# Performance work log

Measured on AMD Instinct MI355X. Metric: run time of the kernel, lower is better.

Reference implementation:

```python
import jax, jax.numpy as jnp
import numpy as np

EMBED_DIM = 1024
NUM_HEADS = 16
HEAD_DIM = EMBED_DIM // NUM_HEADS
B, S = 2, 2048


def setup_inputs() -> dict:
    key = jax.random.key(0)
    ks = jax.random.split(key, 12)
    sd = 1.0 / np.sqrt(EMBED_DIM)
    def lin(kw, kb):
        W = jax.random.uniform(kw, (EMBED_DIM, EMBED_DIM), jnp.float32, -sd, sd)
        b = jax.random.uniform(kb, (EMBED_DIM,), jnp.float32, -sd, sd)
        return W, b
    Wq, bq = lin(ks[0], ks[1])
    Wk, bk = lin(ks[2], ks[3])
    Wv, bv = lin(ks[4], ks[5])
    Wo, bo = lin(ks[6], ks[7])
    q = jax.random.normal(ks[8], (B, S, EMBED_DIM), jnp.float32)
    k = jax.random.normal(ks[9], (B, S, EMBED_DIM), jnp.float32)
    v = jax.random.normal(ks[10], (B, S, EMBED_DIM), jnp.float32)
    # broadcastable causal mask: True = keep (mask==0 positions get -inf)
    attn_mask = jnp.tril(jnp.ones((S, S), jnp.bool_))[None, None]
    return {"q": q, "k": k, "v": v,
            "Wq": Wq, "bq": bq, "Wk": Wk, "bk": bk,
            "Wv": Wv, "bv": bv, "Wo": Wo, "bo": bo,
            "attn_mask": attn_mask}


def reference(q, k, v, Wq, bq, Wk, bk, Wv, bv, Wo, bo, attn_mask):
    bsz, tgt_len, _ = q.shape
    src_len = k.shape[1]
    scale = jnp.sqrt(jnp.float32(HEAD_DIM))
    # projections: PyTorch Linear is x @ W.T + b
    qh = (q @ Wq.T + bq).reshape(bsz, tgt_len, NUM_HEADS, HEAD_DIM).transpose(0, 2, 1, 3)
    kh = (k @ Wk.T + bk).reshape(bsz, src_len, NUM_HEADS, HEAD_DIM).transpose(0, 2, 1, 3)
    vh = (v @ Wv.T + bv).reshape(bsz, src_len, NUM_HEADS, HEAD_DIM).transpose(0, 2, 1, 3)
    # [B,H,T,S] scores
    scores = jnp.einsum('bhtd,bhsd->bhts', qh, kh) / scale
    scores = jnp.where(attn_mask, scores, -jnp.inf)
    attn = jax.nn.softmax(scores, axis=-1)
    out = jnp.einsum('bhts,bhsd->bhtd', attn, vh)  # [B,H,T,D]
    out = out.transpose(0, 2, 1, 3).reshape(bsz, tgt_len, EMBED_DIM)
    return out @ Wo.T + bo
```

## Files before the change

### kernel.cpp

```cpp
#include <hip/hip_runtime.h>
#include <hip/hip_bf16.h>
#include <stdint.h>
#include <stddef.h>

typedef __hip_bfloat16 bf16_t;
typedef __attribute__((ext_vector_type(8))) short short8;
typedef __attribute__((ext_vector_type(4))) short short4v;
typedef __attribute__((ext_vector_type(4))) float floatx4;
typedef __attribute__((ext_vector_type(4))) unsigned uint4v;
typedef __attribute__((ext_vector_type(2))) unsigned uint2v;

#define EMBED 1024
#define NHEAD 16
#define HDIM  64
#define BATCH 2
#define SEQ   2048
#define MTOT  (BATCH*SEQ)
#define NEG_INF (-1e30f)
#define SCALE2 0.18033688011112042f

#define MFMA16(a,b,c) __builtin_amdgcn_mfma_f32_16x16x32_bf16(a,b,c,0,0,0)

static __device__ __forceinline__ short bf16_bits(float x) {
    return __builtin_bit_cast(short, __float2bfloat16(x));
}

static __device__ __forceinline__ float fast_exp2(float x) {
#if __has_builtin(__builtin_amdgcn_exp2f)
    return __builtin_amdgcn_exp2f(x);
#else
    return __expf(x * 0.6931471805599453f);
#endif
}

static __device__ __forceinline__ unsigned pack_bf16x2(float lo, float hi) {
    const unsigned a = (unsigned)(unsigned short)bf16_bits(lo);
    const unsigned b = (unsigned)(unsigned short)bf16_bits(hi);
    return a | (b << 16);
}

static __device__ __forceinline__ void permswap32(unsigned& a, unsigned& b) {
#if __has_builtin(__builtin_amdgcn_permlane32_swap)
    uint2v r = __builtin_amdgcn_permlane32_swap(a, b, false, false);
    a = r[0]; b = r[1];
#else
    asm volatile("v_permlane32_swap_b32 %0, %1" : "+v"(a), "+v"(b));
#endif
}
static __device__ __forceinline__ void permswap16(unsigned& a, unsigned& b) {
#if __has_builtin(__builtin_amdgcn_permlane16_swap)
    uint2v r = __builtin_amdgcn_permlane16_swap(a, b, false, false);
    a = r[0]; b = r[1];
#else
    asm volatile("v_permlane16_swap_b32 %0, %1" : "+v"(a), "+v"(b));
#endif
}

static __device__ __forceinline__ void async_ld16(const bf16_t* g, short* l) {
    __builtin_amdgcn_global_load_lds(
        (const __attribute__((address_space(1))) void*)g,
        (__attribute__((address_space(3))) void*)l,
        16, 0, 0);
}

static __device__ __forceinline__ void store_out(float* p, float v)  { *p = v; }
static __device__ __forceinline__ void store_out(bf16_t* p, float v) { *p = __float2bfloat16(v); }

__global__ __launch_bounds__(256)
void cvt_all(const float* __restrict__ q, const float* __restrict__ k, const float* __restrict__ v,
             const float* __restrict__ wq, const float* __restrict__ wk,
             const float* __restrict__ wv, const float* __restrict__ wo,
             bf16_t* __restrict__ Qx, bf16_t* __restrict__ Kx, bf16_t* __restrict__ Vx,
             bf16_t* __restrict__ Wqb, bf16_t* __restrict__ Wkb,
             bf16_t* __restrict__ Wvb, bf16_t* __restrict__ Wob)
{
    const float* s; bf16_t* d; int n;
    switch (blockIdx.y) {
        case 0:  s = q;  d = Qx;  n = MTOT * EMBED;  break;
        case 1:  s = k;  d = Kx;  n = MTOT * EMBED;  break;
        case 2:  s = v;  d = Vx;  n = MTOT * EMBED;  break;
        case 3:  s = wq; d = Wqb; n = EMBED * EMBED; break;
        case 4:  s = wk; d = Wkb; n = EMBED * EMBED; break;
        case 5:  s = wv; d = Wvb; n = EMBED * EMBED; break;
        default: s = wo; d = Wob; n = EMBED * EMBED; break;
    }
    const int i4 = (int)blockIdx.x * 256 + (int)threadIdx.x;
    if (i4 * 4 < n) {
        const float4 f = ((const float4*)s)[i4];
        short4v o;
        o[0] = bf16_bits(f.x); o[1] = bf16_bits(f.y);
        o[2] = bf16_bits(f.z); o[3] = bf16_bits(f.w);
        ((short4v*)d)[i4] = o;
    }
}

template <typename OutT, bool VT, int BM>
static __device__ __forceinline__ void gemm_tile(
    const bf16_t* __restrict__ A, const bf16_t* __restrict__ W,
    const float* __restrict__ bias, OutT* __restrict__ C, const float scale)
{
    constexpr int MI = BM >> 5;
    constexpr int RPW = BM >> 2;
    const int N = 1024, K = 1024;
    __shared__ alignas(16) short As[BM * 32];
    __shared__ alignas(16) short Bs[128 * 32];

    const int tid  = threadIdx.x;
    const int wave = tid >> 6;
    const int lane = tid & 63;
    const int bm = (int)blockIdx.x >> 3;
    const int bn = (int)blockIdx.x & 7;
    const int m0 = bm * BM, n0 = bn << 7;

    const int wm = ((wave >> 1) & 1) * (BM >> 1);
    const int wn = (wave & 1) << 6;

    floatx4 acc[MI][4] = {};

    const int srowA = wave * RPW + (lane >> 2);
    const int srowB = (wave << 5) + (lane >> 2);
    const int scol  = (lane & 3) << 3;
    const bf16_t* gA = A + (size_t)(m0 + srowA) * K + scol;
    const bf16_t* gB = W + (size_t)(n0 + srowB) * K + scol;
    short* lA0 = &As[wave * RPW * 32];
    short* lA1 = lA0 + 512;
    short* lB0 = &Bs[(wave << 10)];
    short* lB1 = lB0 + 512;

    const int fr = lane & 15;
    const int fk = (lane >> 4) << 3;

    for (int k0 = 0; k0 < K; k0 += 32) {
        __syncthreads();
        async_ld16(gA, lA0);
        if constexpr (BM == 128) async_ld16(gA + (size_t)16 * K, lA1);
        async_ld16(gB, lB0);
        async_ld16(gB + (size_t)16 * K, lB1);
        gA += 32; gB += 32;
        __syncthreads();

        short8 af[MI], bfr[4];
        #pragma unroll
        for (int i = 0; i < MI; ++i)
            af[i] = *(const short8*)&As[(wm + (i << 4) + fr) * 32 + fk];
        #pragma unroll
        for (int j = 0; j < 4; ++j)
            bfr[j] = *(const short8*)&Bs[(wn + (j << 4) + fr) * 32 + fk];
        #pragma unroll
        for (int i = 0; i < MI; ++i)
            #pragma unroll
            for (int j = 0; j < 4; ++j)
                acc[i][j] = MFMA16(af[i], bfr[j], acc[i][j]);
    }

    const int q4 = (lane >> 4) << 2;
    #pragma unroll
    for (int j = 0; j < 4; ++j) {
        const int n = n0 + wn + (j << 4) + fr;
        const float bv = bias[n];
        #pragma unroll
        for (int i = 0; i < MI; ++i) {
            const int mb = m0 + wm + (i << 4) + q4;
            if (VT) {
                const int bb = mb >> 11, ss = mb & 2047;
                short4v pk;
                #pragma unroll
                for (int r = 0; r < 4; ++r)
                    pk[r] = bf16_bits((acc[i][j][r] + bv) * scale);
                *(short4v*)((bf16_t*)C + ((size_t)(bb * 1024 + n) << 11) + ss) = pk;
            } else {
                #pragma unroll
                for (int r = 0; r < 4; ++r)
                    store_out(&C[(size_t)(mb + r) * N + n], (acc[i][j][r] + bv) * scale);
            }
        }
    }
}

__global__ __launch_bounds__(256)
void qkv_proj(const bf16_t* __restrict__ xq, const bf16_t* __restrict__ xk,
              const bf16_t* __restrict__ xv,
              const bf16_t* __restrict__ Wq, const bf16_t* __restrict__ Wk,
              const bf16_t* __restrict__ Wv,
              const float* __restrict__ bq, const float* __restrict__ bk,
              const float* __restrict__ bv,
              bf16_t* __restrict__ Qp, bf16_t* __restrict__ Kp, bf16_t* __restrict__ Vtp)
{
    if (blockIdx.z == 0)      gemm_tile<bf16_t, false, 128>(xq, Wq, bq, Qp, SCALE2);
    else if (blockIdx.z == 1) gemm_tile<bf16_t, false, 128>(xk, Wk, bk, Kp, 1.0f);
    else                      gemm_tile<bf16_t, true , 128>(xv, Wv, bv, Vtp, 1.0f);
}

__global__ __launch_bounds__(256)
void out_proj(const bf16_t* __restrict__ AO, const bf16_t* __restrict__ Wo,
              const float* __restrict__ bo, float* __restrict__ out)
{
    gemm_tile<float, false, 64>(AO, Wo, bo, out, 1.0f);
}

__global__ __launch_bounds__(64)
void attn_causal(const bf16_t* __restrict__ Qp, const bf16_t* __restrict__ Kp,
                 const bf16_t* __restrict__ Vt, bf16_t* __restrict__ AO,
                 float* __restrict__ Op, float* __restrict__ Mp, float* __restrict__ Lp)
{
    const int lane = (int)threadIdx.x & 63;
    const int bid  = (int)blockIdx.x;
    const int bh   = bid & 31;
    const int w    = bid >> 5;
    int tile, sidx, c0, c1;
    bool split;
    if (w < 64) {
        tile  = 63 - (w >> 1);
        sidx  = w & 1;
        split = true;
        const int nch = tile + 1;
        const int h1  = (nch + 1) >> 1;
        c0 = sidx ? h1 : 0;
        c1 = sidx ? nch : h1;
    } else {
        tile  = 95 - w;
        sidx  = 0;
        split = false;
        c0 = 0;
        c1 = tile + 1;
    }
    const bool hasdiag = (c1 == tile + 1);
    const int b = bh >> 4, h = bh & 15;
    const int q0 = tile << 5;

    const int fr   = lane & 15;
    const int quad = lane >> 4;
    const int fk   = quad << 3;

    const bf16_t* Q0 = Qp + (size_t)(b * SEQ + q0 + fr) * EMBED + h * HDIM;
    const short8 aq00 = *(const short8*)(Q0 + fk);
    const short8 aq01 = *(const short8*)(Q0 + 32 + fk);
    const short8 aq10 = *(const short8*)(Q0 + (size_t)16 * EMBED + fk);
    const short8 aq11 = *(const short8*)(Q0 + (size_t)16 * EMBED + 32 + fk);

    const bf16_t* Kbase = Kp + (size_t)(b * SEQ) * EMBED + h * HDIM;
    const bf16_t* Vbase = Vt + ((size_t)(b * 1024 + h * HDIM) << 11);

    floatx4 o0[4] = {}, o1[4] = {};
    float m0 = NEG_INF, m1 = NEG_INF;
    float l0 = 0.f, l1 = 0.f;

    auto smax_pb = [&](const floatx4& sA, const floatx4& sB, float& m_u, float& l_u,
                       floatx4* o_u, const bool diag, const int u16) -> short8 {
        float v0[4], v1[4];
        #pragma unroll
        for (int r = 0; r < 4; ++r) {
            float a  = sA[r];
            float bb = sB[r];
            if (diag) {
                const int kq = (quad << 2) + r;
                const int lq = u16 + fr;
                if (kq > lq)      a  = NEG_INF;
                if (kq + 16 > lq) bb = NEG_INF;
            }
            v0[r] = a; v1[r] = bb;
        }
        float mx = fmaxf(fmaxf(fmaxf(v0[0], v0[1]), fmaxf(v0[2], v0[3])),
                         fmaxf(fmaxf(v1[0], v1[1]), fmaxf(v1[2], v1[3])));
        if (__any(mx > m_u + 8.0f)) {
            mx = fmaxf(mx, __shfl_xor(mx, 16, 64));
            mx = fmaxf(mx, __shfl_xor(mx, 32, 64));
            const float mn = fmaxf(m_u, mx);
            const float al = fast_exp2(m_u - mn);
            m_u = mn;
            l_u *= al;
            #pragma unroll
            for (int t = 0; t < 4; ++t)
                #pragma unroll
                for (int r = 0; r < 4; ++r) o_u[t][r] *= al;
        }
        float ls = 0.f;
        #pragma unroll
        for (int r = 0; r < 4; ++r) {
            v0[r] = fast_exp2(v0[r] - m_u);
            v1[r] = fast_exp2(v1[r] - m_u);
            ls += v0[r] + v1[r];
        }
        l_u += ls;
        unsigned c0p = pack_bf16x2(v0[0], v0[1]);
        unsigned c1p = pack_bf16x2(v0[2], v0[3]);
        unsigned d0p = pack_bf16x2(v1[0], v1[1]);
        unsigned d1p = pack_bf16x2(v1[2], v1[3]);
        permswap32(c0p, d0p);
        permswap32(c1p, d1p);
        permswap16(c0p, d0p);
        permswap16(c1p, d1p);
        uint4v wv; wv[0] = c0p; wv[1] = c1p; wv[2] = d0p; wv[3] = d1p;
        return __builtin_bit_cast(short8, wv);
    };

#define KLOAD(K0_, K1_, K2_, K3_, kvo) do {                                  \
        const bf16_t* Kr0_ = Kbase + (size_t)((kvo) + fr) * EMBED;           \
        const bf16_t* Kr1_ = Kr0_ + (size_t)16 * EMBED;                      \
        K0_ = *(const short8*)(Kr0_ + fk);                                   \
        K1_ = *(const short8*)(Kr0_ + 32 + fk);                              \
        K2_ = *(const short8*)(Kr1_ + fk);                                   \
        K3_ = *(const short8*)(Kr1_ + 32 + fk);                              \
    } while (0)

#define ITER(KC0, KC1, KC2, KC3, KN0, KN1, KN2, KN3, DIAGF, PREF) do {       \
        const int kv0 = c << 5;                                              \
         \
        const short8 vf0 = *(const short8*)(Vbase + ((size_t)(fr)      << 11) + kv0 + fk); \
        const short8 vf1 = *(const short8*)(Vbase + ((size_t)(16 + fr) << 11) + kv0 + fk); \
        const short8 vf2 = *(const short8*)(Vbase + ((size_t)(32 + fr) << 11) + kv0 + fk); \
        const short8 vf3 = *(const short8*)(Vbase + ((size_t)(48 + fr) << 11) + kv0 + fk); \
        if (PREF) { KLOAD(KN0, KN1, KN2, KN3, kv0 + 32); }                   \
        floatx4 s00 = {}, s01 = {}, s10 = {}, s11 = {};                      \
        s00 = MFMA16(KC0, aq00, s00); s00 = MFMA16(KC1, aq01, s00);          \
        s10 = MFMA16(KC0, aq10, s10); s10 = MFMA16(KC1, aq11, s10);          \
        s01 = MFMA16(KC2, aq00, s01); s01 = MFMA16(KC3, aq01, s01);          \
        s11 = MFMA16(KC2, aq10, s11); s11 = MFMA16(KC3, aq11, s11);          \
        const short8 pb0 = smax_pb(s00, s01, m0, l0, o0, DIAGF, 0);          \
        const short8 pb1 = smax_pb(s10, s11, m1, l1, o1, DIAGF, 16);         \
        o0[0] = MFMA16(vf0, pb0, o0[0]); o1[0] = MFMA16(vf0, pb1, o1[0]);    \
        o0[1] = MFMA16(vf1, pb0, o0[1]); o1[1] = MFMA16(vf1, pb1, o1[1]);    \
        o0[2] = MFMA16(vf2, pb0, o0[2]); o1[2] = MFMA16(vf2, pb1, o1[2]);    \
        o0[3] = MFMA16(vf3, pb0, o0[3]); o1[3] = MFMA16(vf3, pb1, o1[3]);    \
    } while (0)

    short8 ka0, ka1, ka2, ka3, kb0, kb1, kb2, kb3;
    KLOAD(ka0, ka1, ka2, ka3, c0 << 5);

    int c = c0;
    const int cl = c1 - 1;
    if (cl > c0) {
        for (;;) {
            ITER(ka0, ka1, ka2, ka3, kb0, kb1, kb2, kb3, false, true);
            if (++c == cl) break;
            ITER(kb0, kb1, kb2, kb3, ka0, ka1, ka2, ka3, false, true);
            if (++c == cl) break;
        }
    }
    if ((c - c0) & 1) { ITER(kb0, kb1, kb2, kb3, ka0, ka1, ka2, ka3, hasdiag, false); }
    else              { ITER(ka0, ka1, ka2, ka3, kb0, kb1, kb2, kb3, hasdiag, false); }

#undef ITER
#undef KLOAD

    { float t = __shfl_xor(l0, 16, 64); l0 += t; t = __shfl_xor(l0, 32, 64); l0 += t; }
    { float t = __shfl_xor(l1, 16, 64); l1 += t; t = __shfl_xor(l1, 32, 64); l1 += t; }

    if (!split) {
        const float i0 = 1.0f / l0;
        const float i1 = 1.0f / l1;
        bf16_t* out0 = AO + (size_t)(b * SEQ + q0 + fr) * EMBED + h * HDIM + (quad << 2);
        bf16_t* out1 = out0 + (size_t)16 * EMBED;
        #pragma unroll
        for (int t = 0; t < 4; ++t) {
            short4v pk0, pk1;
            #pragma unroll
            for (int r = 0; r < 4; ++r) {
                pk0[r] = bf16_bits(o0[t][r] * i0);
                pk1[r] = bf16_bits(o1[t][r] * i1);
            }
            *(short4v*)(out0 + (t << 4)) = pk0;
            *(short4v*)(out1 + (t << 4)) = pk1;
        }
    } else {
        const int p = (bh << 5) | (tile - 32);
        float* Ob = Op + (((size_t)sidx << 10) + p) * 2048;
        #pragma unroll
        for (int t = 0; t < 4; ++t) {
            *(floatx4*)&Ob[fr * 64 + (t << 4) + (quad << 2)]        = o0[t];
            *(floatx4*)&Ob[(16 + fr) * 64 + (t << 4) + (quad << 2)] = o1[t];
        }
        if (quad == 0) {
            const size_t mb = (((size_t)sidx << 10) + p) * 32;
            Mp[mb + fr]      = m0;
            Mp[mb + 16 + fr] = m1;
            Lp[mb + fr]      = l0;
            Lp[mb + 16 + fr] = l1;
        }
    }
}

__global__ __launch_bounds__(256)
void attn_combine(const float* __restrict__ Op, const float* __restrict__ Mp,
                  const float* __restrict__ Lp, bf16_t* __restrict__ AO)
{
    const int p   = (int)blockIdx.x;
    const int tid = (int)threadIdx.x;
    const int row = tid >> 3;
    const int d0  = (tid & 7) << 3;
    const int bh = p >> 5, tile = 32 + (p & 31);
    const int b = bh >> 4, h = bh & 15;

    const float m0 = Mp[(size_t)p * 32 + row];
    const float m1 = Mp[(size_t)(1024 + p) * 32 + row];
    const float l0 = Lp[(size_t)p * 32 + row];
    const float l1 = Lp[(size_t)(1024 + p) * 32 + row];
    const float M  = fmaxf(m0, m1);
    const float w0 = fast_exp2(m0 - M);
    const float w1 = fast_exp2(m1 - M);
    const float rd = 1.0f / (l0 * w0 + l1 * w1);

    const float* O0 = Op + ((size_t)p << 11) + row * 64 + d0;
    const float* O1 = O0 + ((size_t)1024 << 11);
    const float4 a0 = *(const float4*)O0;
    const float4 a1 = *(const float4*)(O0 + 4);
    const float4 c0 = *(const float4*)O1;
    const float4 c1 = *(const float4*)(O1 + 4);

    short8 pk;
    pk[0] = bf16_bits((a0.x * w0 + c0.x * w1) * rd);
    pk[1] = bf16_bits((a0.y * w0 + c0.y * w1) * rd);
    pk[2] = bf16_bits((a0.z * w0 + c0.z * w1) * rd);
    pk[3] = bf16_bits((a0.w * w0 + c0.w * w1) * rd);
    pk[4] = bf16_bits((a1.x * w0 + c1.x * w1) * rd);
    pk[5] = bf16_bits((a1.y * w0 + c1.y * w1) * rd);
    pk[6] = bf16_bits((a1.z * w0 + c1.z * w1) * rd);
    pk[7] = bf16_bits((a1.w * w0 + c1.w * w1) * rd);
    *(short8*)(AO + (size_t)(b * SEQ + tile * 32 + row) * EMBED + h * HDIM + d0) = pk;
}

extern "C" void kernel_launch(void* const* d_in, const int* in_sizes, int n_in,
                              void* d_out, int out_size, void* d_ws, size_t ws_size,
                              hipStream_t stream)
{
    (void)in_sizes; (void)n_in; (void)out_size; (void)ws_size;
    const float* q  = (const float*)d_in[0];
    const float* k  = (const float*)d_in[1];
    const float* v  = (const float*)d_in[2];
    const float* Wq = (const float*)d_in[3];
    const float* bq = (const float*)d_in[4];
    const float* Wk = (const float*)d_in[5];
    const float* bk = (const float*)d_in[6];
    const float* Wv = (const float*)d_in[7];
    const float* bv = (const float*)d_in[8];
    const float* Wo = (const float*)d_in[9];
    const float* bo = (const float*)d_in[10];

    const size_t NX = (size_t)MTOT * EMBED;
    const size_t NW = (size_t)EMBED * EMBED;
    bf16_t* Qx  = (bf16_t*)d_ws;
    bf16_t* Kx  = Qx  + NX;
    bf16_t* Vx  = Kx  + NX;
    bf16_t* Wqb = Vx  + NX;
    bf16_t* Wkb = Wqb + NW;
    bf16_t* Wvb = Wkb + NW;
    bf16_t* Wob = Wvb + NW;
    bf16_t* Qp  = Wob + NW;
    bf16_t* Kp  = Qp  + NX;
    bf16_t* Vtp = Kp  + NX;
    bf16_t* AO  = Vtp + NX;

    float* Op = (float*)Qx;
    float* Mp = (float*)Wqb;
    float* Lp = Mp + 2 * 1024 * 32;

    dim3 blk(256);
    cvt_all<<<dim3(4096, 7), blk, 0, stream>>>(q, k, v, Wq, Wk, Wv, Wo,
                                               Qx, Kx, Vx, Wqb, Wkb, Wvb, Wob);
    qkv_proj<<<dim3(256, 1, 3), blk, 0, stream>>>(Qx, Kx, Vx, Wqb, Wkb, Wvb,
                                                  bq, bk, bv, Qp, Kp, Vtp);
    attn_causal<<<dim3(3072), dim3(64), 0, stream>>>(Qp, Kp, Vtp, AO, Op, Mp, Lp);
    attn_combine<<<dim3(1024), blk, 0, stream>>>(Op, Mp, Lp, AO);
    out_proj<<<dim3(512), blk, 0, stream>>>(AO, Wob, bo, (float*)d_out);
}
```

Before: 284.1 us.

## Enlarge attention query tile to 64 rows and process 64-wide K steps in GEMM

The causal attention kernel now handles 64 query rows per wave instead of 32, so each K/V fragment load is reused across four 16-row groups. The split/unsplit work distribution, the diagonal masking (now two masked chunks) and the combine kernel are reworked to match. The GEMM tile loads two 32-wide K slices per barrier pair, which halves the number of synchronisations. The attention kernel also gets a launch-bounds occupancy hint. The trade-off is higher register pressure (16 accumulators per wave) and half as many attention blocks, which can reduce parallelism.

```diff
diff --git a/kernel.cpp b/kernel.cpp
--- a/kernel.cpp
+++ b/kernel.cpp
@@ -99,11 +99,11 @@
     const bf16_t* __restrict__ A, const bf16_t* __restrict__ W,
     const float* __restrict__ bias, OutT* __restrict__ C, const float scale)
 {
-    constexpr int MI = BM >> 5;
+    constexpr int MI  = BM >> 5;
     constexpr int RPW = BM >> 2;
     const int N = 1024, K = 1024;
-    __shared__ alignas(16) short As[BM * 32];
-    __shared__ alignas(16) short Bs[128 * 32];
+    __shared__ alignas(16) short As[2][BM * 32];
+    __shared__ alignas(16) short Bs[2][128 * 32];
 
     const int tid  = threadIdx.x;
     const int wave = tid >> 6;
@@ -122,35 +122,44 @@
     const int scol  = (lane & 3) << 3;
     const bf16_t* gA = A + (size_t)(m0 + srowA) * K + scol;
     const bf16_t* gB = W + (size_t)(n0 + srowB) * K + scol;
-    short* lA0 = &As[wave * RPW * 32];
-    short* lA1 = lA0 + 512;
-    short* lB0 = &Bs[(wave << 10)];
-    short* lB1 = lB0 + 512;
 
     const int fr = lane & 15;
     const int fk = (lane >> 4) << 3;
 
-    for (int k0 = 0; k0 < K; k0 += 32) {
+    for (int k0 = 0; k0 < K; k0 += 64) {
         __syncthreads();
-        async_ld16(gA, lA0);
-        if constexpr (BM == 128) async_ld16(gA + (size_t)16 * K, lA1);
-        async_ld16(gB, lB0);
-        async_ld16(gB + (size_t)16 * K, lB1);
-        gA += 32; gB += 32;
+        short* a0 = &As[0][wave * RPW * 32];
+        short* a1 = &As[1][wave * RPW * 32];
+        short* b0 = &Bs[0][wave << 10];
+        short* b1 = &Bs[1][wave << 10];
+        async_ld16(gA,      a0);
+        async_ld16(gA + 32, a1);
+        if constexpr (BM == 128) {
+            async_ld16(gA + (size_t)16 * K,      a0 + 512);
+            async_ld16(gA + (size_t)16 * K + 32, a1 + 512);
+        }
+        async_ld16(gB,      b0);
+        async_ld16(gB + 32, b1);
+        async_ld16(gB + (size_t)16 * K,      b0 + 512);
+        async_ld16(gB + (size_t)16 * K + 32, b1 + 512);
+        gA += 64; gB += 64;
         __syncthreads();
 
-        short8 af[MI], bfr[4];
         #pragma unroll
-        for (int i = 0; i < MI; ++i)
-            af[i] = *(const short8*)&As[(wm + (i << 4) + fr) * 32 + fk];
-        #pragma unroll
-        for (int j = 0; j < 4; ++j)
-            bfr[j] = *(const short8*)&Bs[(wn + (j << 4) + fr) * 32 + fk];
-        #pragma unroll
-        for (int i = 0; i < MI; ++i)
+        for (int hh = 0; hh < 2; ++hh) {
+            short8 af[MI], bfr[4];
+            #pragma unroll
+            for (int i = 0; i < MI; ++i)
+                af[i] = *(const short8*)&As[hh][(wm + (i << 4) + fr) * 32 + fk];
             #pragma unroll
             for (int j = 0; j < 4; ++j)
-                acc[i][j] = MFMA16(af[i], bfr[j], acc[i][j]);
+                bfr[j] = *(const short8*)&Bs[hh][(wn + (j << 4) + fr) * 32 + fk];
+            #pragma unroll
+            for (int i = 0; i < MI; ++i)
+                #pragma unroll
+                for (int j = 0; j < 4; ++j)
+                    acc[i][j] = MFMA16(af[i], bfr[j], acc[i][j]);
+        }
     }
 
     const int q4 = (lane >> 4) << 2;
@@ -198,7 +207,7 @@
     gemm_tile<float, false, 64>(AO, Wo, bo, out, 1.0f);
 }
 
-__global__ __launch_bounds__(64)
+__global__ __launch_bounds__(64, 2)
 void attn_causal(const bf16_t* __restrict__ Qp, const bf16_t* __restrict__ Kp,
                  const bf16_t* __restrict__ Vt, bf16_t* __restrict__ AO,
                  float* __restrict__ Op, float* __restrict__ Mp, float* __restrict__ Lp)
@@ -207,58 +216,60 @@
     const int bid  = (int)blockIdx.x;
     const int bh   = bid & 31;
     const int w    = bid >> 5;
+    const int g    = w / 3, r3 = w - g * 3;
     int tile, sidx, c0, c1;
     bool split;
-    if (w < 64) {
-        tile  = 63 - (w >> 1);
-        sidx  = w & 1;
+    if (r3 < 2) {
+        tile  = 31 - g;
+        sidx  = r3;
         split = true;
-        const int nch = tile + 1;
-        const int h1  = (nch + 1) >> 1;
+        const int nch = 2 * tile + 2;
+        const int h1  = nch >> 1;
         c0 = sidx ? h1 : 0;
         c1 = sidx ? nch : h1;
     } else {
-        tile  = 95 - w;
+        tile  = 15 - g;
         sidx  = 0;
         split = false;
         c0 = 0;
-        c1 = tile + 1;
-    }
-    const bool hasdiag = (c1 == tile + 1);
+        c1 = 2 * tile + 2;
+    }
+    const bool hasdiag = (c1 == 2 * tile + 2);
     const int b = bh >> 4, h = bh & 15;
-    const int q0 = tile << 5;
+    const int q0 = tile << 6;
 
     const int fr   = lane & 15;
     const int quad = lane >> 4;
     const int fk   = quad << 3;
 
-    const bf16_t* Q0 = Qp + (size_t)(b * SEQ + q0 + fr) * EMBED + h * HDIM;
-    const short8 aq00 = *(const short8*)(Q0 + fk);
-    const short8 aq01 = *(const short8*)(Q0 + 32 + fk);
-    const short8 aq10 = *(const short8*)(Q0 + (size_t)16 * EMBED + fk);
-    const short8 aq11 = *(const short8*)(Q0 + (size_t)16 * EMBED + 32 + fk);
+    const bf16_t* Qb = Qp + (size_t)(b * SEQ + q0 + fr) * EMBED + h * HDIM;
+    short8 aq[4][2];
+    #pragma unroll
+    for (int u = 0; u < 4; ++u) {
+        aq[u][0] = *(const short8*)(Qb + (size_t)(u * 16) * EMBED + fk);
+        aq[u][1] = *(const short8*)(Qb + (size_t)(u * 16) * EMBED + 32 + fk);
+    }
 
     const bf16_t* Kbase = Kp + (size_t)(b * SEQ) * EMBED + h * HDIM;
     const bf16_t* Vbase = Vt + ((size_t)(b * 1024 + h * HDIM) << 11);
 
-    floatx4 o0[4] = {}, o1[4] = {};
-    float m0 = NEG_INF, m1 = NEG_INF;
-    float l0 = 0.f, l1 = 0.f;
+    floatx4 o[4][4] = {};
+    float m[4] = {NEG_INF, NEG_INF, NEG_INF, NEG_INF};
+    float l[4] = {};
 
     auto smax_pb = [&](const floatx4& sA, const floatx4& sB, float& m_u, float& l_u,
-                       floatx4* o_u, const bool diag, const int u16) -> short8 {
+                       floatx4* o_u, const bool masked, const int off) -> short8 {
         float v0[4], v1[4];
         #pragma unroll
-        for (int r = 0; r < 4; ++r) {
-            float a  = sA[r];
-            float bb = sB[r];
-            if (diag) {
-                const int kq = (quad << 2) + r;
-                const int lq = u16 + fr;
-                if (kq > lq)      a  = NEG_INF;
-                if (kq + 16 > lq) bb = NEG_INF;
+        for (int rr = 0; rr < 4; ++rr) {
+            float a  = sA[rr];
+            float bb = sB[rr];
+            if (masked) {
+                const int kq = (quad << 2) + rr;
+                if (kq > off + fr)      a  = NEG_INF;
+                if (kq + 16 > off + fr) bb = NEG_INF;
             }
-            v0[r] = a; v1[r] = bb;
+            v0[rr] = a; v1[rr] = bb;
         }
         float mx = fmaxf(fmaxf(fmaxf(v0[0], v0[1]), fmaxf(v0[2], v0[3])),
                          fmaxf(fmaxf(v1[0], v1[1]), fmaxf(v1[2], v1[3])));
@@ -272,14 +283,14 @@
             #pragma unroll
             for (int t = 0; t < 4; ++t)
                 #pragma unroll
-                for (int r = 0; r < 4; ++r) o_u[t][r] *= al;
+                for (int rr = 0; rr < 4; ++rr) o_u[t][rr] *= al;
         }
         float ls = 0.f;
         #pragma unroll
-        for (int r = 0; r < 4; ++r) {
-            v0[r] = fast_exp2(v0[r] - m_u);
-            v1[r] = fast_exp2(v1[r] - m_u);
-            ls += v0[r] + v1[r];
+        for (int rr = 0; rr < 4; ++rr) {
+            v0[rr] = fast_exp2(v0[rr] - m_u);
+            v1[rr] = fast_exp2(v1[rr] - m_u);
+            ls += v0[rr] + v1[rr];
         }
         l_u += ls;
         unsigned c0p = pack_bf16x2(v0[0], v0[1]);
@@ -303,79 +314,99 @@
         K3_ = *(const short8*)(Kr1_ + 32 + fk);                              \
     } while (0)
 
-#define ITER(KC0, KC1, KC2, KC3, KN0, KN1, KN2, KN3, DIAGF, PREF) do {       \
-        const int kv0 = c << 5;                                              \
-         \
-        const short8 vf0 = *(const short8*)(Vbase + ((size_t)(fr)      << 11) + kv0 + fk); \
-        const short8 vf1 = *(const short8*)(Vbase + ((size_t)(16 + fr) << 11) + kv0 + fk); \
-        const short8 vf2 = *(const short8*)(Vbase + ((size_t)(32 + fr) << 11) + kv0 + fk); \
-        const short8 vf3 = *(const short8*)(Vbase + ((size_t)(48 + fr) << 11) + kv0 + fk); \
+#define ITER(KC0, KC1, KC2, KC3, KN0, KN1, KN2, KN3, CC, MASKED, OFFB, PREF) do { \
+        const int kv0 = (CC) << 5;                                           \
+        short8 vf[4];                                                        \
+        _Pragma("unroll")                                                    \
+        for (int t = 0; t < 4; ++t)                                          \
+            vf[t] = *(const short8*)(Vbase + ((size_t)((t << 4) + fr) << 11) + kv0 + fk); \
         if (PREF) { KLOAD(KN0, KN1, KN2, KN3, kv0 + 32); }                   \
-        floatx4 s00 = {}, s01 = {}, s10 = {}, s11 = {};                      \
-        s00 = MFMA16(KC0, aq00, s00); s00 = MFMA16(KC1, aq01, s00);          \
-        s10 = MFMA16(KC0, aq10, s10); s10 = MFMA16(KC1, aq11, s10);          \
-        s01 = MFMA16(KC2, aq00, s01); s01 = MFMA16(KC3, aq01, s01);          \
-        s11 = MFMA16(KC2, aq10, s11); s11 = MFMA16(KC3, aq11, s11);          \
-        const short8 pb0 = smax_pb(s00, s01, m0, l0, o0, DIAGF, 0);          \
-        const short8 pb1 = smax_pb(s10, s11, m1, l1, o1, DIAGF, 16);         \
-        o0[0] = MFMA16(vf0, pb0, o0[0]); o1[0] = MFMA16(vf0, pb1, o1[0]);    \
-        o0[1] = MFMA16(vf1, pb0, o0[1]); o1[1] = MFMA16(vf1, pb1, o1[1]);    \
-        o0[2] = MFMA16(vf2, pb0, o0[2]); o1[2] = MFMA16(vf2, pb1, o1[2]);    \
-        o0[3] = MFMA16(vf3, pb0, o0[3]); o1[3] = MFMA16(vf3, pb1, o1[3]);    \
+        floatx4 s0[4], s1[4];                                                \
+        _Pragma("unroll")                                                    \
+        for (int u = 0; u < 4; ++u) {                                        \
+            floatx4 z0 = {}, z1 = {};                                        \
+            z0 = MFMA16(KC0, aq[u][0], z0); z0 = MFMA16(KC1, aq[u][1], z0);  \
+            z1 = MFMA16(KC2, aq[u][0], z1); z1 = MFMA16(KC3, aq[u][1], z1);  \
+            s0[u] = z0; s1[u] = z1;                                          \
+        }                                                                    \
+        short8 pb[4];                                                        \
+        _Pragma("unroll")                                                    \
+        for (int u = 0; u < 4; ++u)                                          \
+            pb[u] = smax_pb(s0[u], s1[u], m[u], l[u], o[u], MASKED, u * 16 + (OFFB)); \
+        _Pragma("unroll")                                                    \
+        for (int u = 0; u < 4; ++u)                                          \
+            _Pragma("unroll")                                                \
+            for (int t = 0; t < 4; ++t)                                      \
+                o[u][t] = MFMA16(vf[t], pb[u], o[u][t]);                     \
     } while (0)
 
     short8 ka0, ka1, ka2, ka3, kb0, kb1, kb2, kb3;
     KLOAD(ka0, ka1, ka2, ka3, c0 << 5);
 
     int c = c0;
-    const int cl = c1 - 1;
-    if (cl > c0) {
+    const int cm = c1 - (hasdiag ? 2 : 1);
+    if (cm > c0) {
         for (;;) {
-            ITER(ka0, ka1, ka2, ka3, kb0, kb1, kb2, kb3, false, true);
-            if (++c == cl) break;
-            ITER(kb0, kb1, kb2, kb3, ka0, ka1, ka2, ka3, false, true);
-            if (++c == cl) break;
-        }
-    }
-    if ((c - c0) & 1) { ITER(kb0, kb1, kb2, kb3, ka0, ka1, ka2, ka3, hasdiag, false); }
-    else              { ITER(ka0, ka1, ka2, ka3, kb0, kb1, kb2, kb3, hasdiag, false); }
+            ITER(ka0, ka1, ka2, ka3, kb0, kb1, kb2, kb3, c, false, 0, true);
+            if (++c == cm) break;
+            ITER(kb0, kb1, kb2, kb3, ka0, ka1, ka2, ka3, c, false, 0, true);
+            if (++c == cm) break;
+        }
+    }
+    const bool ina = (((c - c0) & 1) == 0);
+    if (hasdiag) {
+        if (ina) {
+            ITER(ka0, ka1, ka2, ka3, kb0, kb1, kb2, kb3, c,     true,   0, true);
+            ITER(kb0, kb1, kb2, kb3, ka0, ka1, ka2, ka3, c + 1, true, -32, false);
+        } else {
+            ITER(kb0, kb1, kb2, kb3, ka0, ka1, ka2, ka3, c,     true,   0, true);
+            ITER(ka0, ka1, ka2, ka3, kb0, kb1, kb2, kb3, c + 1, true, -32, false);
+        }
+    } else {
+        if (ina) ITER(ka0, ka1, ka2, ka3, kb0, kb1, kb2, kb3, c, false, 0, false);
+        else     ITER(kb0, kb1, kb2, kb3, ka0, ka1, ka2, ka3, c, false, 0, false);
+    }
 
 #undef ITER
 #undef KLOAD
 
-    { float t = __shfl_xor(l0, 16, 64); l0 += t; t = __shfl_xor(l0, 32, 64); l0 += t; }
-    { float t = __shfl_xor(l1, 16, 64); l1 += t; t = __shfl_xor(l1, 32, 64); l1 += t; }
+    #pragma unroll
+    for (int u = 0; u < 4; ++u) {
+        float t = __shfl_xor(l[u], 16, 64); l[u] += t;
+        t = __shfl_xor(l[u], 32, 64);       l[u] += t;
+    }
 
     if (!split) {
-        const float i0 = 1.0f / l0;
-        const float i1 = 1.0f / l1;
-        bf16_t* out0 = AO + (size_t)(b * SEQ + q0 + fr) * EMBED + h * HDIM + (quad << 2);
-        bf16_t* out1 = out0 + (size_t)16 * EMBED;
         #pragma unroll
-        for (int t = 0; t < 4; ++t) {
-            short4v pk0, pk1;
-            #pragma unroll
-            for (int r = 0; r < 4; ++r) {
-                pk0[r] = bf16_bits(o0[t][r] * i0);
-                pk1[r] = bf16_bits(o1[t][r] * i1);
+        for (int u = 0; u < 4; ++u) {
+            const float iu = 1.0f / l[u];
+            bf16_t* outp = AO + (size_t)(b * SEQ + q0 + u * 16 + fr) * EMBED
+                              + h * HDIM + (quad << 2);
+            #pragma unroll
+            for (int t = 0; t < 4; ++t) {
+                short4v pk;
+                #pragma unroll
+                for (int rr = 0; rr < 4; ++rr)
+                    pk[rr] = bf16_bits(o[u][t][rr] * iu);
+                *(short4v*)(outp + (t << 4)) = pk;
             }
-            *(short4v*)(out0 + (t << 4)) = pk0;
-            *(short4v*)(out1 + (t << 4)) = pk1;
         }
     } else {
-        const int p = (bh << 5) | (tile - 32);
-        float* Ob = Op + (((size_t)sidx << 10) + p) * 2048;
+        const int p = (bh << 4) | (tile - 16);
+        float* Ob = Op + ((size_t)(sidx * 512 + p)) * 4096;
         #pragma unroll
-        for (int t = 0; t < 4; ++t) {
-            *(floatx4*)&Ob[fr * 64 + (t << 4) + (quad << 2)]        = o0[t];
-            *(floatx4*)&Ob[(16 + fr) * 64 + (t << 4) + (quad << 2)] = o1[t];
+        for (int u = 0; u < 4; ++u) {
+            #pragma unroll
+            for (int t = 0; t < 4; ++t)
+                *(floatx4*)&Ob[(u * 16 + fr) * 64 + (t << 4) + (quad << 2)] = o[u][t];
         }
         if (quad == 0) {
-            const size_t mb = (((size_t)sidx << 10) + p) * 32;
-            Mp[mb + fr]      = m0;
-            Mp[mb + 16 + fr] = m1;
-            Lp[mb + fr]      = l0;
-            Lp[mb + 16 + fr] = l1;
+            const size_t mb = (size_t)(sidx * 512 + p) * 64;
+            #pragma unroll
+            for (int u = 0; u < 4; ++u) {
+                Mp[mb + u * 16 + fr] = m[u];
+                Lp[mb + u * 16 + fr] = l[u];
+            }
         }
     }
 }
@@ -386,37 +417,41 @@
 {
     const int p   = (int)blockIdx.x;
     const int tid = (int)threadIdx.x;
-    const int row = tid >> 3;
-    const int d0  = (tid & 7) << 3;
-    const int bh = p >> 5, tile = 32 + (p & 31);
+    const int row = tid >> 2;
+    const int d0  = (tid & 3) << 4;
+    const int bh = p >> 4, tile = 16 + (p & 15);
     const int b = bh >> 4, h = bh & 15;
 
-    const float m0 = Mp[(size_t)p * 32 + row];
-    const float m1 = Mp[(size_t)(1024 + p) * 32 + row];
-    const float l0 = Lp[(size_t)p * 32 + row];
-    const float l1 = Lp[(size_t)(1024 + p) * 32 + row];
+    const float m0 = Mp[(size_t)p * 64 + row];
+    const float m1 = Mp[(size_t)(512 + p) * 64 + row];
+    const float l0 = Lp[(size_t)p * 64 + row];
+    const float l1 = Lp[(size_t)(512 + p) * 64 + row];
     const float M  = fmaxf(m0, m1);
     const float w0 = fast_exp2(m0 - M);
     const float w1 = fast_exp2(m1 - M);
     const float rd = 1.0f / (l0 * w0 + l1 * w1);
 
-    const float* O0 = Op + ((size_t)p << 11) + row * 64 + d0;
-    const float* O1 = O0 + ((size_t)1024 << 11);
-    const float4 a0 = *(const float4*)O0;
-    const float4 a1 = *(const float4*)(O0 + 4);
-    const float4 c0 = *(const float4*)O1;
-    const float4 c1 = *(const float4*)(O1 + 4);
-
-    short8 pk;
-    pk[0] = bf16_bits((a0.x * w0 + c0.x * w1) * rd);
-    pk[1] = bf16_bits((a0.y * w0 + c0.y * w1) * rd);
-    pk[2] = bf16_bits((a0.z * w0 + c0.z * w1) * rd);
-    pk[3] = bf16_bits((a0.w * w0 + c0.w * w1) * rd);
-    pk[4] = bf16_bits((a1.x * w0 + c1.x * w1) * rd);
-    pk[5] = bf16_bits((a1.y * w0 + c1.y * w1) * rd);
-    pk[6] = bf16_bits((a1.z * w0 + c1.z * w1) * rd);
-    pk[7] = bf16_bits((a1.w * w0 + c1.w * w1) * rd);
-    *(short8*)(AO + (size_t)(b * SEQ + tile * 32 + row) * EMBED + h * HDIM + d0) = pk;
+    const float* O0 = Op + (size_t)p * 4096 + row * 64 + d0;
+    const float* O1 = O0 + (size_t)512 * 4096;
+    bf16_t* outp = AO + (size_t)(b * SEQ + tile * 64 + row) * EMBED + h * HDIM + d0;
+
+    #pragma unroll
+    for (int seg = 0; seg < 2; ++seg) {
+        const float4 a0 = *(const float4*)(O0 + seg * 8);
+        const float4 a1 = *(const float4*)(O0 + seg * 8 + 4);
+        const float4 c0 = *(const float4*)(O1 + seg * 8);
+        const float4 c1 = *(const float4*)(O1 + seg * 8 + 4);
+        short8 pk;
+        pk[0] = bf16_bits((a0.x * w0 + c0.x * w1) * rd);
+        pk[1] = bf16_bits((a0.y * w0 + c0.y * w1) * rd);
+        pk[2] = bf16_bits((a0.z * w0 + c0.z * w1) * rd);
+        pk[3] = bf16_bits((a0.w * w0 + c0.w * w1) * rd);
+        pk[4] = bf16_bits((a1.x * w0 + c1.x * w1) * rd);
+        pk[5] = bf16_bits((a1.y * w0 + c1.y * w1) * rd);
+        pk[6] = bf16_bits((a1.z * w0 + c1.z * w1) * rd);
+        pk[7] = bf16_bits((a1.w * w0 + c1.w * w1) * rd);
+        *(short8*)(outp + seg * 8) = pk;
+    }
 }
 
 extern "C" void kernel_launch(void* const* d_in, const int* in_sizes, int n_in,
@@ -452,14 +487,14 @@
 
     float* Op = (float*)Qx;
     float* Mp = (float*)Wqb;
-    float* Lp = Mp + 2 * 1024 * 32;
+    float* Lp = Mp + 2 * 512 * 64;
 
     dim3 blk(256);
     cvt_all<<<dim3(4096, 7), blk, 0, stream>>>(q, k, v, Wq, Wk, Wv, Wo,
                                                Qx, Kx, Vx, Wqb, Wkb, Wvb, Wob);
     qkv_proj<<<dim3(256, 1, 3), blk, 0, stream>>>(Qx, Kx, Vx, Wqb, Wkb, Wvb,
                                                   bq, bk, bv, Qp, Kp, Vtp);
-    attn_causal<<<dim3(3072), dim3(64), 0, stream>>>(Qp, Kp, Vtp, AO, Op, Mp, Lp);
-    attn_combine<<<dim3(1024), blk, 0, stream>>>(Op, Mp, Lp, AO);
+    attn_causal<<<dim3(1536), dim3(64), 0, stream>>>(Qp, Kp, Vtp, AO, Op, Mp, Lp);
+    attn_combine<<<dim3(512), blk, 0, stream>>>(Op, Mp, Lp, AO);
     out_proj<<<dim3(512), blk, 0, stream>>>(AO, Wob, bo, (float*)d_out);
 }
```

New measurement: 261.4 us. -8.0%, faster.
